# Optimization experiments

Hardware: AMD Instinct MI355X
Metric: run time of the kernel (lower is better)

The kernel has to match this reference:

```python
import jax, jax.numpy as jnp
import numpy as np

N, E = 50000, 1600000
IN, OUT, H = 128, 32, 2
NT, ET = 20, 4
ETE, EAE, ED = 16, 16, 16
SLOPE = 0.2  # conv_neg_slope


def setup_inputs() -> dict:
    key = jax.random.key(0)
    ks = jax.random.split(key, 11)
    d_att = 2 * OUT + ETE + EAE
    return dict(
        x=jax.random.normal(ks[0], (N, IN), jnp.float32),
        edge_index=jax.random.randint(ks[1], (2, E), 0, N),
        ntypes=jax.random.randint(ks[2], (N,), 0, NT),
        etypes=jax.random.randint(ks[3], (E,), 0, ET),
        eattr=jax.random.normal(ks[4], (E, ED), jnp.float32),
        het_W=jax.random.normal(ks[5], (NT, IN, OUT), jnp.float32) / np.sqrt(IN).astype(np.float32),
        het_b=jnp.zeros((NT, OUT), jnp.float32),
        etype_table=jax.random.normal(ks[6], (ET, ETE), jnp.float32),
        eattr_W=jax.random.normal(ks[7], (ED, EAE), jnp.float32) / np.sqrt(ED).astype(np.float32),
        att_W=jax.random.normal(ks[8], (d_att, H), jnp.float32) / np.sqrt(d_att).astype(np.float32),
        lin_W=jax.random.normal(ks[9], (OUT + EAE, OUT), jnp.float32) / np.sqrt(OUT + EAE).astype(np.float32),
    )


def _lrelu(v):
    return jax.nn.leaky_relu(v, SLOPE)


def _heat_conv(x, edge_index, ntypes, etypes, eattr,
               het_W, het_b, etype_table, eattr_W, att_W, lin_W):
    # HeteroLinear: node-type-conditioned linear transform (loop over 20 types,
    # avoids materializing a [N, IN, OUT] gathered-weight tensor)
    h = jnp.zeros((x.shape[0], het_W.shape[-1]), x.dtype)
    for t in range(het_W.shape[0]):
        h = h + jnp.where((ntypes == t)[:, None], x @ het_W[t] + het_b[t], 0.0)

    src, dst = edge_index[0], edge_index[1]
    ete = _lrelu(etype_table[etypes])        # [E, ETE] edge-type embedding
    ea = _lrelu(eattr @ eattr_W)             # [E, EAE] edge-attr embedding
    x_i = h[dst]                             # target node feats [E, OUT]
    x_j = h[src]                             # source node feats [E, OUT]

    feat = jnp.concatenate([x_i, x_j, ete, ea], axis=-1)
    alpha = _lrelu(feat @ att_W)             # [E, H] raw attention logits

    # softmax grouped by destination node, per head
    amax = jax.ops.segment_max(alpha, dst, num_segments=N)  # [N, H]
    alpha = jnp.exp(alpha - amax[dst])
    denom = jax.ops.segment_sum(alpha, dst, num_segments=N)  # [N, H]
    alpha = alpha / denom[dst]

    msg = jnp.concatenate([x_j, ea], axis=-1) @ lin_W        # [E, OUT]
    m = (msg[:, None, :] * alpha[:, :, None]).reshape(alpha.shape[0], H * OUT)
    out = jax.ops.segment_sum(m, dst, num_segments=N)        # [N, H*OUT]
    return out  # concat=True -> flattened heads


def reference(x, edge_index, ntypes, etypes, eattr,
              het_W, het_b, etype_table, eattr_W, att_W, lin_W):
    out = _heat_conv(x, edge_index, ntypes, etypes, eattr,
                     het_W, het_b, etype_table, eattr_W, att_W, lin_W)
    return jax.nn.relu(out)  # final activation in forward (eval mode: no dropout)
```

## Files before the change

### kernel.cpp

```cpp
#include <hip/hip_runtime.h>
#include <hip/hip_fp16.h>

#define NN 50000
#define EE 1600000
#define IN_F 128
#define SLOPE 0.2f
#define NB_SCAN 196
#define NSHARD 8
#define NB_NODE 1563
#define NB_CNT  6250
#define NB_FUSE (NB_NODE + NB_CNT)

typedef _Float16 hf2 __attribute__((ext_vector_type(2)));
typedef float f4 __attribute__((ext_vector_type(4)));

#define NTL(p) __builtin_nontemporal_load(p)

static __device__ __forceinline__ float4 ntl4(const float* p) {
    f4 v = __builtin_nontemporal_load((const f4*)p);
    return make_float4(v.x, v.y, v.z, v.w);
}

__global__ __launch_bounds__(256) void k_node_count(
    const float* __restrict__ x, const int* __restrict__ ntypes,
    const float* __restrict__ hetW, const float* __restrict__ hetb,
    const float* __restrict__ linW, const float* __restrict__ attW,
    __half* __restrict__ hlinH, float* __restrict__ auxS,
    float* __restrict__ auxD,
    const int* __restrict__ dst, int* __restrict__ cnt8,
    unsigned* __restrict__ rankpack)
{
    int b = blockIdx.x;
    int tid = threadIdx.x;
    if (b % 5 != 0) {
        int cid = b - b / 5 - 1;
        int e = cid * 256 + tid;
        int d = NTL(dst + e);
        unsigned xcc;
        asm volatile("s_getreg_b32 %0, hwreg(HW_REG_XCC_ID)" : "=s"(xcc));
        int sh = xcc & (NSHARD - 1);
        int lr = atomicAdd(&cnt8[sh * NN + d], 1);
        rankpack[e] = ((unsigned)lr << 3) | (unsigned)sh;
        return;
    }
    int nb = b / 5;
    __shared__ float sH[32 * 33];
    __shared__ float sLin[32 * 32];
    for (int i = tid; i < 1024; i += 256) sLin[i] = linW[i];

    int g = tid >> 3;
    int j = tid & 7;
    int n = nb * 32 + g;
    int nc = n < NN ? n : NN - 1;
    int t = ntypes[nc];
    const float* W = hetW + (size_t)t * (IN_F * 32);
    const float* xr = x + (size_t)nc * IN_F;

    float4 acc = ((const float4*)(hetb + t * 32))[j];
    #pragma unroll 4
    for (int c = 0; c < 32; ++c) {
        float4 xv = ntl4(xr + 4 * c);
        const float* Wr = W + (4 * c) * 32 + 4 * j;
        float4 w0 = *(const float4*)(Wr);
        float4 w1 = *(const float4*)(Wr + 32);
        float4 w2 = *(const float4*)(Wr + 64);
        float4 w3 = *(const float4*)(Wr + 96);
        acc.x += xv.x * w0.x + xv.y * w1.x + xv.z * w2.x + xv.w * w3.x;
        acc.y += xv.x * w0.y + xv.y * w1.y + xv.z * w2.y + xv.w * w3.y;
        acc.z += xv.x * w0.z + xv.y * w1.z + xv.z * w2.z + xv.w * w3.z;
        acc.w += xv.x * w0.w + xv.y * w1.w + xv.z * w2.w + xv.w * w3.w;
    }
    sH[g * 33 + 4 * j + 0] = acc.x;
    sH[g * 33 + 4 * j + 1] = acc.y;
    sH[g * 33 + 4 * j + 2] = acc.z;
    sH[g * 33 + 4 * j + 3] = acc.w;
    __syncthreads();

    int o = tid & 31;
    #pragma unroll
    for (int pass = 0; pass < 4; ++pass) {
        int g2 = (tid >> 5) + 8 * pass;
        int n2 = nb * 32 + g2;
        if (n2 >= NN) break;
        float accl = 0.0f;
        #pragma unroll
        for (int k = 0; k < 32; ++k)
            accl += sH[g2 * 33 + k] * sLin[k * 32 + o];
        hlinH[(size_t)n2 * 32 + o] = __float2half_rn(accl);

        float hv = sH[g2 * 33 + o];
        float p0 = hv * attW[o * 2],        p1 = hv * attW[o * 2 + 1];
        float p2 = hv * attW[(32 + o) * 2], p3 = hv * attW[(32 + o) * 2 + 1];
        #pragma unroll
        for (int m = 16; m >= 1; m >>= 1) {
            p0 += __shfl_xor(p0, m, 32);
            p1 += __shfl_xor(p1, m, 32);
            p2 += __shfl_xor(p2, m, 32);
            p3 += __shfl_xor(p3, m, 32);
        }
        if (o == 0) {
            auxD[n2 * 2] = p0; auxD[n2 * 2 + 1] = p1;
            auxS[n2 * 2] = p2; auxS[n2 * 2 + 1] = p3;
        }
    }
}

__global__ __launch_bounds__(256) void k_scanA(
    const int* __restrict__ cnt8, int* __restrict__ offsets,
    int* __restrict__ bsum, int* __restrict__ sb8)
{
    __shared__ int s[256];
    int t = threadIdx.x;
    int i = blockIdx.x * 256 + t;
    int tot = 0;
    if (i < NN) {
        int pre = 0;
        #pragma unroll
        for (int sh = 0; sh < NSHARD; ++sh) {
            int c = cnt8[sh * NN + i];
            sb8[sh * NN + i] = pre;
            pre += c;
        }
        tot = pre;
    }
    s[t] = tot;
    __syncthreads();
    for (int off = 1; off < 256; off <<= 1) {
        int v = (t >= off) ? s[t - off] : 0;
        __syncthreads();
        s[t] += v;
        __syncthreads();
    }
    if (i < NN) offsets[i] = s[t] - tot;
    if (t == 255) bsum[blockIdx.x] = s[255];
}

__global__ __launch_bounds__(256) void k_scanB(
    const int* __restrict__ bsum, int* __restrict__ bbase,
    const float* __restrict__ etab, const float* __restrict__ attW,
    float* __restrict__ etedot)
{
    __shared__ int s[256];
    int t = threadIdx.x;
    if (t < 8) {
        int et = t >> 1, hh = t & 1;
        float acc = 0.0f;
        for (int k = 0; k < 16; ++k) {
            float v = etab[et * 16 + k];
            v = v > 0.0f ? v : SLOPE * v;
            acc += v * attW[(64 + k) * 2 + hh];
        }
        etedot[t] = acc;
    }
    int c = (t < NB_SCAN) ? bsum[t] : 0;
    s[t] = c;
    __syncthreads();
    for (int off = 1; off < 256; off <<= 1) {
        int v = (t >= off) ? s[t - off] : 0;
        __syncthreads();
        s[t] += v;
        __syncthreads();
    }
    if (t < NB_SCAN) bbase[t] = s[t] - c;
}

__global__ __launch_bounds__(256) void k_scanC(
    int* __restrict__ offsets, const int* __restrict__ bbase,
    int* __restrict__ sb8)
{
    int t = threadIdx.x;
    int i = blockIdx.x * 256 + t;
    if (i < NN) {
        int v = offsets[i] + bbase[blockIdx.x];
        offsets[i] = v;
        #pragma unroll
        for (int sh = 0; sh < NSHARD; ++sh)
            sb8[sh * NN + i] += v;
    }
    if (i == 0) offsets[NN] = EE;
}

__global__ __launch_bounds__(256) void k_pre6(
    const int* __restrict__ srcp, const int* __restrict__ dstp,
    const int* __restrict__ etypes, const float* __restrict__ eattr,
    const float* __restrict__ eaW, const float* __restrict__ attW,
    const float* __restrict__ etedot, const float* __restrict__ auxS,
    const float* __restrict__ auxD, const unsigned* __restrict__ rankpack,
    const int* __restrict__ sb8, float4* __restrict__ recBuf)
{
    int e = blockIdx.x * 256 + threadIdx.x;
    int s = NTL(srcp + e);
    int d = NTL(dstp + e);
    int et = NTL(etypes + e);
    unsigned rp = NTL(rankpack + e);
    int slot = sb8[(size_t)(rp & 7) * NN + d] + (int)(rp >> 3);

    float attr[16];
    {
        const float* ap = eattr + (size_t)e * 16;
        #pragma unroll
        for (int q = 0; q < 4; ++q) {
            float4 v = ntl4(ap + 4 * q);
            attr[4*q+0] = v.x; attr[4*q+1] = v.y;
            attr[4*q+2] = v.z; attr[4*q+3] = v.w;
        }
    }
    float ea[16];
    #pragma unroll
    for (int j = 0; j < 16; ++j) {
        float acc = 0.0f;
        #pragma unroll
        for (int k = 0; k < 16; ++k) acc += attr[k] * eaW[k * 16 + j];
        ea[j] = acc > 0.0f ? acc : SLOPE * acc;
    }

    float2 aD = ((const float2*)auxD)[d];
    float2 aS = ((const float2*)auxS)[s];
    float2 eD = ((const float2*)etedot)[et];
    float al0 = aD.x + aS.x + eD.x;
    float al1 = aD.y + aS.y + eD.y;
    #pragma unroll
    for (int j = 0; j < 16; ++j) {
        al0 += ea[j] * attW[(80 + j) * 2];
        al1 += ea[j] * attW[(80 + j) * 2 + 1];
    }
    al0 = al0 > 0.0f ? al0 : SLOPE * al0;
    al1 = al1 > 0.0f ? al1 : SLOPE * al1;
    float p0 = __expf(al0), p1 = __expf(al1);

    __half2 eh[8];
    #pragma unroll
    for (int q = 0; q < 8; ++q)
        eh[q] = __floats2half2_rn(ea[2*q], ea[2*q+1]);

    float4* P = recBuf + (size_t)slot * 4;
    P[0] = ((const float4*)eh)[0];
    P[1] = ((const float4*)eh)[1];
    union { float4 v; int i[4]; float f[4]; } mu;
    mu.i[0] = s; mu.f[1] = p0; mu.f[2] = p1; mu.i[3] = 0;
    P[2] = mu.v;
    P[3] = make_float4(0.f, 0.f, 0.f, 0.f);
}

__global__ __launch_bounds__(256) void k_gather6(
    const int* __restrict__ offsets, const float4* __restrict__ recBuf,
    const __half* __restrict__ hlinH, const float* __restrict__ linW,
    float* __restrict__ out)
{
    int tid = blockIdx.x * 256 + threadIdx.x;
    int n = tid >> 6;
    int lane = threadIdx.x & 63;
    if (n >= NN) return;
    int o = lane & 31, hh = lane >> 5, j = o & 15;

    int s0 = __builtin_amdgcn_readfirstlane(offsets[n]);
    int s1 = __builtin_amdgcn_readfirstlane(offsets[n + 1]);

    const char* base = (const char*)recBuf;
    float accm = 0.0f, accp = 0.0f, wacc = 0.0f;

    int slot = s0;
    for (; slot + 3 < s1; slot += 4) {
        const char* r0 = base + ((size_t)(slot + 0) << 6);
        const char* r1 = base + ((size_t)(slot + 1) << 6);
        const char* r2 = base + ((size_t)(slot + 2) << 6);
        const char* r3 = base + ((size_t)(slot + 3) << 6);
        int4 m0 = *(const int4*)(r0 + 32);
        int4 m1 = *(const int4*)(r1 + 32);
        int4 m2 = *(const int4*)(r2 + 32);
        int4 m3 = *(const int4*)(r3 + 32);
        float e0 = __half2float(*(const __half*)(r0 + 2 * j));
        float e1 = __half2float(*(const __half*)(r1 + 2 * j));
        float e2 = __half2float(*(const __half*)(r2 + 2 * j));
        float e3 = __half2float(*(const __half*)(r3 + 2 * j));
        float hv0 = __half2float(hlinH[(size_t)m0.x * 32 + o]);
        float hv1 = __half2float(hlinH[(size_t)m1.x * 32 + o]);
        float hv2 = __half2float(hlinH[(size_t)m2.x * 32 + o]);
        float hv3 = __half2float(hlinH[(size_t)m3.x * 32 + o]);
        float p0 = __int_as_float(hh ? m0.z : m0.y);
        float p1 = __int_as_float(hh ? m1.z : m1.y);
        float p2 = __int_as_float(hh ? m2.z : m2.y);
        float p3 = __int_as_float(hh ? m3.z : m3.y);
        accm += p0 * hv0;
        accm += p1 * hv1;
        accm += p2 * hv2;
        accm += p3 * hv3;
        wacc += p0 * e0;
        wacc += p1 * e1;
        wacc += p2 * e2;
        wacc += p3 * e3;
        accp += (p0 + p1) + (p2 + p3);
    }
    for (; slot < s1; ++slot) {
        const char* r = base + ((size_t)slot << 6);
        int4 m = *(const int4*)(r + 32);
        float e = __half2float(*(const __half*)(r + 2 * j));
        float hv = __half2float(hlinH[(size_t)m.x * 32 + o]);
        float p = __int_as_float(hh ? m.z : m.y);
        accm += p * hv;
        wacc += p * e;
        accp += p;
    }

    float elin = 0.0f;
    int bsel = lane & 32;
    #pragma unroll
    for (int jj = 0; jj < 16; ++jj) {
        float wv = __shfl(wacc, bsel | jj, 64);
        elin += wv * linW[(32 + jj) * 32 + o];
    }
    float num = accm + elin;
    float v = accp > 0.0f ? num / accp : 0.0f;
    __builtin_nontemporal_store(v > 0.0f ? v : 0.0f, out + (size_t)n * 64 + lane);
}

extern "C" void kernel_launch(void* const* d_in, const int* in_sizes, int n_in,
                              void* d_out, int out_size, void* d_ws, size_t ws_size,
                              hipStream_t stream)
{
    const float* x      = (const float*)d_in[0];
    const int*   eidx   = (const int*)  d_in[1];
    const int*   ntypes = (const int*)  d_in[2];
    const int*   etypes = (const int*)  d_in[3];
    const float* eattr  = (const float*)d_in[4];
    const float* hetW   = (const float*)d_in[5];
    const float* hetb   = (const float*)d_in[6];
    const float* etab   = (const float*)d_in[7];
    const float* eaW    = (const float*)d_in[8];
    const float* attW   = (const float*)d_in[9];
    const float* linW   = (const float*)d_in[10];
    float* out = (float*)d_out;

    char* ws = (char*)d_ws;
    size_t off = 0;
    auto alloc = [&](size_t bytes) {
        char* p = ws + off;
        off = (off + bytes + 255) & ~(size_t)255;
        return p;
    };
    __half*   hlinH    = (__half*)  alloc((size_t)NN * 32 * sizeof(__half));
    float*    auxS     = (float*)   alloc((size_t)NN * 2 * sizeof(float));
    float*    auxD     = (float*)   alloc((size_t)NN * 2 * sizeof(float));
    float*    etedot   = (float*)   alloc(8 * sizeof(float));
    int*      cnt8     = (int*)     alloc((size_t)NSHARD * NN * sizeof(int));
    int*      offsets  = (int*)     alloc(((size_t)NN + 1) * sizeof(int));
    int*      sb8      = (int*)     alloc((size_t)NSHARD * NN * sizeof(int));
    unsigned* rankpack = (unsigned*)alloc((size_t)EE * sizeof(unsigned));
    int*      bsum     = (int*)     alloc(256 * sizeof(int));
    int*      bbase    = (int*)     alloc(256 * sizeof(int));
    float4*   recBuf   = (float4*)  alloc((size_t)EE * 64);
    (void)ws_size;

    const int* srcp = eidx;
    const int* dstp = eidx + EE;

    hipMemsetAsync(cnt8, 0, (size_t)NSHARD * NN * sizeof(int), stream);

    k_node_count<<<NB_FUSE, 256, 0, stream>>>(x, ntypes, hetW, hetb, linW,
                                              attW, hlinH, auxS, auxD,
                                              dstp, cnt8, rankpack);
    k_scanA<<<NB_SCAN, 256, 0, stream>>>(cnt8, offsets, bsum, sb8);
    k_scanB<<<1, 256, 0, stream>>>(bsum, bbase, etab, attW, etedot);
    k_scanC<<<NB_SCAN, 256, 0, stream>>>(offsets, bbase, sb8);
    k_pre6<<<EE / 256, 256, 0, stream>>>(srcp, dstp, etypes, eattr, eaW, attW,
                                         etedot, auxS, auxD, rankpack, sb8,
                                         recBuf);
    k_gather6<<<(NN * 64 + 255) / 256, 256, 0, stream>>>(offsets, recBuf,
                                                         hlinH, linW, out);
}
```

Measured before the change: 454.0 us.

## Sort nodes by type before hetero linear, coarsen edge counting, pack aux into float4

Two new kernels build a type histogram and a type-sorted node list, so each 32-node block in the hetero-linear stage uses mostly one weight matrix and reads it coherently from cache. The edge-counting blocks now handle four edges each, interleaved one-to-one with node blocks, which reduces the block count. The separate src/dst attention-term arrays are merged into a single float4 per node so k_pre6 does one vector load per endpoint. The cost is two extra small launches, a scattered write pattern for hlinH/aux, and atomics on global type counters.

```diff
diff --git a/kernel.cpp b/kernel.cpp
--- a/kernel.cpp
+++ b/kernel.cpp
@@ -7,8 +7,9 @@
 #define SLOPE 0.2f
 #define NB_SCAN 196
 #define NSHARD 8
+#define NLPAD 50016
 #define NB_NODE 1563
-#define NB_CNT  6250
+#define NB_CNT 1563
 #define NB_FUSE (NB_NODE + NB_CNT)
 
 typedef _Float16 hf2 __attribute__((ext_vector_type(2)));
@@ -21,38 +22,89 @@
     return make_float4(v.x, v.y, v.z, v.w);
 }
 
+__global__ __launch_bounds__(256) void k_typehist(
+    const int* __restrict__ ntypes, int* __restrict__ gtype)
+{
+    __shared__ int lcnt[32];
+    int tid = threadIdx.x;
+    if (tid < 32) lcnt[tid] = 0;
+    __syncthreads();
+    int i = blockIdx.x * 256 + tid;
+    if (i < NN) atomicAdd(&lcnt[ntypes[i]], 1);
+    __syncthreads();
+    if (tid < 20 && lcnt[tid]) atomicAdd(&gtype[tid], lcnt[tid]);
+}
+
+__global__ __launch_bounds__(256) void k_typescatter(
+    const int* __restrict__ ntypes, const int* __restrict__ gtype,
+    int* __restrict__ gclaim, int* __restrict__ nodeList)
+{
+    __shared__ int lcnt[32];
+    __shared__ int lbase[32];
+    int tid = threadIdx.x;
+    if (tid < 32) lcnt[tid] = 0;
+    __syncthreads();
+    int i = blockIdx.x * 256 + tid;
+    int t = 0, lr = 0;
+    bool valid = i < NN;
+    if (valid) { t = ntypes[i]; lr = atomicAdd(&lcnt[t], 1); }
+    __syncthreads();
+    if (tid < 20) lbase[tid] = atomicAdd(&gclaim[tid], lcnt[tid]);
+    __syncthreads();
+    if (valid) {
+        int base = 0;
+        for (int u = 0; u < t; ++u) base += gtype[u];
+        nodeList[base + lbase[t] + lr] = (t << 16) | i;
+    } else if (i < NLPAD) {
+        int tl = ntypes[NN - 1];
+        nodeList[i] = (tl << 16) | (NN - 1);
+    }
+}
+
 __global__ __launch_bounds__(256) void k_node_count(
-    const float* __restrict__ x, const int* __restrict__ ntypes,
+    const float* __restrict__ x, const int* __restrict__ nodeList,
     const float* __restrict__ hetW, const float* __restrict__ hetb,
     const float* __restrict__ linW, const float* __restrict__ attW,
-    __half* __restrict__ hlinH, float* __restrict__ auxS,
-    float* __restrict__ auxD,
+    __half* __restrict__ hlinH, float4* __restrict__ aux4,
     const int* __restrict__ dst, int* __restrict__ cnt8,
     unsigned* __restrict__ rankpack)
 {
     int b = blockIdx.x;
     int tid = threadIdx.x;
-    if (b % 5 != 0) {
-        int cid = b - b / 5 - 1;
-        int e = cid * 256 + tid;
-        int d = NTL(dst + e);
+    if (b & 1) {
+        int cid = b >> 1;
         unsigned xcc;
         asm volatile("s_getreg_b32 %0, hwreg(HW_REG_XCC_ID)" : "=s"(xcc));
         int sh = xcc & (NSHARD - 1);
-        int lr = atomicAdd(&cnt8[sh * NN + d], 1);
-        rankpack[e] = ((unsigned)lr << 3) | (unsigned)sh;
+        int e0 = cid * 1024 + tid;
+        int e1 = e0 + 256, e2 = e0 + 512, e3 = e0 + 768;
+        bool v1 = e1 < EE, v2 = e2 < EE, v3 = e3 < EE;
+        int d0 = NTL(dst + e0);
+        int d1 = v1 ? NTL(dst + e1) : 0;
+        int d2 = v2 ? NTL(dst + e2) : 0;
+        int d3 = v3 ? NTL(dst + e3) : 0;
+        int r0 = atomicAdd(&cnt8[sh * NN + d0], 1);
+        int r1 = v1 ? atomicAdd(&cnt8[sh * NN + d1], 1) : 0;
+        int r2 = v2 ? atomicAdd(&cnt8[sh * NN + d2], 1) : 0;
+        int r3 = v3 ? atomicAdd(&cnt8[sh * NN + d3], 1) : 0;
+        rankpack[e0] = ((unsigned)r0 << 3) | (unsigned)sh;
+        if (v1) rankpack[e1] = ((unsigned)r1 << 3) | (unsigned)sh;
+        if (v2) rankpack[e2] = ((unsigned)r2 << 3) | (unsigned)sh;
+        if (v3) rankpack[e3] = ((unsigned)r3 << 3) | (unsigned)sh;
         return;
     }
-    int nb = b / 5;
+    int nb = b >> 1;
     __shared__ float sH[32 * 33];
     __shared__ float sLin[32 * 32];
+    __shared__ int sNid[32];
     for (int i = tid; i < 1024; i += 256) sLin[i] = linW[i];
 
     int g = tid >> 3;
     int j = tid & 7;
-    int n = nb * 32 + g;
-    int nc = n < NN ? n : NN - 1;
-    int t = ntypes[nc];
+    int packed = nodeList[nb * 32 + g];
+    int nc = packed & 0xFFFF;
+    int t = packed >> 16;
+    if (j == 0) sNid[g] = nc;
     const float* W = hetW + (size_t)t * (IN_F * 32);
     const float* xr = x + (size_t)nc * IN_F;
 
@@ -80,13 +132,12 @@
     #pragma unroll
     for (int pass = 0; pass < 4; ++pass) {
         int g2 = (tid >> 5) + 8 * pass;
-        int n2 = nb * 32 + g2;
-        if (n2 >= NN) break;
+        int pn = sNid[g2];
         float accl = 0.0f;
         #pragma unroll
         for (int k = 0; k < 32; ++k)
             accl += sH[g2 * 33 + k] * sLin[k * 32 + o];
-        hlinH[(size_t)n2 * 32 + o] = __float2half_rn(accl);
+        hlinH[(size_t)pn * 32 + o] = __float2half_rn(accl);
 
         float hv = sH[g2 * 33 + o];
         float p0 = hv * attW[o * 2],        p1 = hv * attW[o * 2 + 1];
@@ -98,10 +149,7 @@
             p2 += __shfl_xor(p2, m, 32);
             p3 += __shfl_xor(p3, m, 32);
         }
-        if (o == 0) {
-            auxD[n2 * 2] = p0; auxD[n2 * 2 + 1] = p1;
-            auxS[n2 * 2] = p2; auxS[n2 * 2 + 1] = p3;
-        }
+        if (o == 0) aux4[pn] = make_float4(p0, p1, p2, p3);
     }
 }
 
@@ -184,9 +232,9 @@
     const int* __restrict__ srcp, const int* __restrict__ dstp,
     const int* __restrict__ etypes, const float* __restrict__ eattr,
     const float* __restrict__ eaW, const float* __restrict__ attW,
-    const float* __restrict__ etedot, const float* __restrict__ auxS,
-    const float* __restrict__ auxD, const unsigned* __restrict__ rankpack,
-    const int* __restrict__ sb8, float4* __restrict__ recBuf)
+    const float* __restrict__ etedot, const float4* __restrict__ aux4,
+    const unsigned* __restrict__ rankpack, const int* __restrict__ sb8,
+    float4* __restrict__ recBuf)
 {
     int e = blockIdx.x * 256 + threadIdx.x;
     int s = NTL(srcp + e);
@@ -214,11 +262,11 @@
         ea[j] = acc > 0.0f ? acc : SLOPE * acc;
     }
 
-    float2 aD = ((const float2*)auxD)[d];
-    float2 aS = ((const float2*)auxS)[s];
+    float4 aD = aux4[d];
+    float4 aS = aux4[s];
     float2 eD = ((const float2*)etedot)[et];
-    float al0 = aD.x + aS.x + eD.x;
-    float al1 = aD.y + aS.y + eD.y;
+    float al0 = aD.x + aS.z + eD.x;
+    float al1 = aD.y + aS.w + eD.y;
     #pragma unroll
     for (int j = 0; j < 16; ++j) {
         al0 += ea[j] * attW[(80 + j) * 2];
@@ -339,13 +387,16 @@
         return p;
     };
     __half*   hlinH    = (__half*)  alloc((size_t)NN * 32 * sizeof(__half));
-    float*    auxS     = (float*)   alloc((size_t)NN * 2 * sizeof(float));
-    float*    auxD     = (float*)   alloc((size_t)NN * 2 * sizeof(float));
+    float4*   aux4     = (float4*)  alloc((size_t)NN * sizeof(float4));
     float*    etedot   = (float*)   alloc(8 * sizeof(float));
-    int*      cnt8     = (int*)     alloc((size_t)NSHARD * NN * sizeof(int));
+    int*      cnts     = (int*)     alloc(((size_t)NSHARD * NN + 64) * sizeof(int));
+    int*      cnt8     = cnts;
+    int*      gtype    = cnts + (size_t)NSHARD * NN;
+    int*      gclaim   = gtype + 20;
     int*      offsets  = (int*)     alloc(((size_t)NN + 1) * sizeof(int));
     int*      sb8      = (int*)     alloc((size_t)NSHARD * NN * sizeof(int));
     unsigned* rankpack = (unsigned*)alloc((size_t)EE * sizeof(unsigned));
+    int*      nodeList = (int*)     alloc((size_t)NLPAD * sizeof(int));
     int*      bsum     = (int*)     alloc(256 * sizeof(int));
     int*      bbase    = (int*)     alloc(256 * sizeof(int));
     float4*   recBuf   = (float4*)  alloc((size_t)EE * 64);
@@ -354,16 +405,18 @@
     const int* srcp = eidx;
     const int* dstp = eidx + EE;
 
-    hipMemsetAsync(cnt8, 0, (size_t)NSHARD * NN * sizeof(int), stream);
-
-    k_node_count<<<NB_FUSE, 256, 0, stream>>>(x, ntypes, hetW, hetb, linW,
-                                              attW, hlinH, auxS, auxD,
+    hipMemsetAsync(cnts, 0, ((size_t)NSHARD * NN + 64) * sizeof(int), stream);
+
+    k_typehist<<<NB_SCAN, 256, 0, stream>>>(ntypes, gtype);
+    k_typescatter<<<NB_SCAN, 256, 0, stream>>>(ntypes, gtype, gclaim, nodeList);
+    k_node_count<<<NB_FUSE, 256, 0, stream>>>(x, nodeList, hetW, hetb, linW,
+                                              attW, hlinH, aux4,
                                               dstp, cnt8, rankpack);
     k_scanA<<<NB_SCAN, 256, 0, stream>>>(cnt8, offsets, bsum, sb8);
     k_scanB<<<1, 256, 0, stream>>>(bsum, bbase, etab, attW, etedot);
     k_scanC<<<NB_SCAN, 256, 0, stream>>>(offsets, bbase, sb8);
     k_pre6<<<EE / 256, 256, 0, stream>>>(srcp, dstp, etypes, eattr, eaW, attW,
-                                         etedot, auxS, auxD, rankpack, sb8,
+                                         etedot, aux4, rankpack, sb8,
                                          recBuf);
     k_gather6<<<(NN * 64 + 255) / 256, 256, 0, stream>>>(offsets, recBuf,
                                                          hlinH, linW, out);
```

New measurement: 458.2 us. Within noise of the previous version (+0.9%).
